# Performance work log

Measured on AMD Instinct MI355X. Metric: run time of the kernel, lower is better.

The kernel has to match this reference:

```python
import jax, jax.numpy as jnp
import numpy as np

PC_MIN = jnp.array([0.0, -39.68, -3.0], jnp.float32)
VOX = jnp.array([0.16, 0.16, 4.0], jnp.float32)
NX, NY = 432, 496  # grid cells in x and y (z grid size is 1)
MAXP = 32          # max points per pillar


def setup_inputs():
    key = jax.random.key(0)
    ks = jax.random.split(key, 16)
    B, N = 2, 16000
    u = jax.random.uniform(ks[0], (B, N, 4), dtype=jnp.float32)
    # points uniformly spread over the point-cloud range, intensity in [0,1)
    points = jnp.stack([u[..., 0] * 69.12, u[..., 1] * 79.36 - 39.68,
                        u[..., 2] * 4.0 - 3.0, u[..., 3]], axis=-1)

    def cw(k, co, ci):
        return jax.random.normal(k, (co, ci, 3, 3), jnp.float32) / np.float32(np.sqrt(ci * 9.0))

    def cws(k, L, c):
        return jax.random.normal(k, (L, c, c, 3, 3), jnp.float32) / np.float32(np.sqrt(c * 9.0))

    def st(k, shape):
        k1, k2 = jax.random.split(k)
        return (1.0 + 0.1 * jax.random.normal(k1, shape, jnp.float32),
                0.1 * jax.random.normal(k2, shape, jnp.float32))

    vfe_w = 0.1 * jax.random.normal(ks[1], (64, 10), jnp.float32)
    vfe_s, vfe_t = st(ks[2], (64,))
    b1_w0 = cw(ks[3], 4, 64);   b1_s0, b1_t0 = st(ks[4], (4,))
    b1_w = cws(ks[5], 3, 4);    b1_s, b1_t = st(ks[6], (3, 4))
    b2_w0 = cw(ks[7], 16, 4);   b2_s0, b2_t0 = st(ks[8], (16,))
    b2_w = cws(ks[9], 5, 16);   b2_s, b2_t = st(ks[10], (5, 16))
    b3_w0 = cw(ks[11], 64, 16); b3_s0, b3_t0 = st(ks[12], (64,))
    b3_w = cws(ks[13], 5, 64);  b3_s, b3_t = st(ks[14], (5, 64))
    return dict(points=points, vfe_w=vfe_w, vfe_s=vfe_s, vfe_t=vfe_t,
                b1_w0=b1_w0, b1_s0=b1_s0, b1_t0=b1_t0, b1_w=b1_w, b1_s=b1_s, b1_t=b1_t,
                b2_w0=b2_w0, b2_s0=b2_s0, b2_t0=b2_t0, b2_w=b2_w, b2_s=b2_s, b2_t=b2_t,
                b3_w0=b3_w0, b3_s0=b3_s0, b3_t0=b3_t0, b3_w=b3_w, b3_s=b3_s, b3_t=b3_t)


def _voxelize_vfe_scatter(points, vfe_w, vfe_s, vfe_t):
    """Hard voxelization (hash-bucket by pillar coord, pad to MAXP) + PillarVFE + scatter to BEV canvas."""
    B, N, C = points.shape
    V = B * N  # worst case: every point its own pillar
    pts = points.reshape(V, C)
    cid = jnp.floor((pts[:, :3] - PC_MIN) / VOX).astype(jnp.int32)
    cid = jnp.clip(cid, 0, jnp.array([NX - 1, NY - 1, 0], jnp.int32))
    bidx = jnp.repeat(jnp.arange(B, dtype=jnp.int32), N)
    # linear pillar id: b*NY*NX + y*NX + x  (z grid dim is 1 -> z idx always 0)
    gid = bidx * (NY * NX) + cid[:, 1] * NX + cid[:, 0]
    order = jnp.argsort(gid)  # stable -> preserves per-pillar point order
    g = gid[order]; p = pts[order]; c = cid[order]
    pos = jnp.arange(V, dtype=jnp.int32)
    flag = jnp.concatenate([jnp.ones((1,), bool), g[1:] != g[:-1]])
    vidx = jnp.cumsum(flag) - 1                                 # dense pillar index
    rank = pos - jax.lax.cummax(jnp.where(flag, pos, 0), axis=0)  # slot within pillar
    keep = rank < MAXP
    voxels = jnp.zeros((V, MAXP, C), points.dtype).at[vidx, rank].set(p, mode='drop')
    num = jnp.zeros((V,), jnp.int32).at[vidx].add(keep.astype(jnp.int32))
    OOB = B * NY * NX
    pillar_gid = jnp.full((V,), OOB, jnp.int32).at[vidx].set(g)  # unused slots stay out-of-bounds
    pillar_c = jnp.zeros((V, 3), jnp.int32).at[vidx].set(c)
    # PillarVFE features: [x,y,z,r, cluster offset(3), center offset(3)] = 10
    denom = jnp.maximum(num, 1).astype(points.dtype)[:, None]
    mean = jnp.zeros((V, 3), points.dtype).at[vidx].add(p[:, :3] * keep[:, None]) / denom
    f_cluster = voxels[:, :, :3] - mean[:, None, :]
    center = pillar_c.astype(points.dtype) * VOX + (VOX * 0.5 + PC_MIN)
    f_center = voxels[:, :, :3] - center[:, None, :]
    mask = (jnp.arange(MAXP)[None, :] < num[:, None])[:, :, None].astype(points.dtype)
    feat = jnp.concatenate([voxels, f_cluster, f_center], axis=-1) * mask  # (V, 32, 10)
    x = jnp.einsum('vpc,oc->vpo', feat, vfe_w)        # PFN linear (no bias)
    x = jax.nn.relu(x * vfe_s + vfe_t)                # eval-mode BN folded to scale/shift
    pillar = x.max(axis=1)                            # (V, 64) max over points
    canvas = jnp.zeros((B * NY * NX, 64), points.dtype).at[pillar_gid].set(pillar, mode='drop')
    return canvas.reshape(B, NY, NX, 64).transpose(0, 3, 1, 2)  # (B, 64, NY, NX)


def _conv_bn_relu(x, w, s, t):
    y = jax.lax.conv_general_dilated(x, w, (1, 1), [(1, 1), (1, 1)],
                                     dimension_numbers=('NCHW', 'OIHW', 'NCHW'))
    return jax.nn.relu(y * s[None, :, None, None] + t[None, :, None, None])


def _block(x, w0, s0, t0, ws, ss, ts):
    x = _conv_bn_relu(x, w0, s0, t0)
    for i in range(ws.shape[0]):  # fixed small layer count
        x = _conv_bn_relu(x, ws[i], ss[i], ts[i])
    return x


def reference(points, vfe_w, vfe_s, vfe_t,
              b1_w0, b1_s0, b1_t0, b1_w, b1_s, b1_t,
              b2_w0, b2_s0, b2_t0, b2_w, b2_s, b2_t,
              b3_w0, b3_s0, b3_t0, b3_w, b3_s, b3_t):
    bev = _voxelize_vfe_scatter(points, vfe_w, vfe_s, vfe_t)
    x1 = _block(bev, b1_w0, b1_s0, b1_t0, b1_w, b1_s, b1_t)
    x2 = _block(x1, b2_w0, b2_s0, b2_t0, b2_w, b2_s, b2_t)
    x3 = _block(x2, b3_w0, b3_s0, b3_t0, b3_w, b3_s, b3_t)
    # no deblocks (cfg lacks UPSAMPLE_STRIDES) -> concat raw block outputs: 4+16+64 = 84 ch
    return jnp.concatenate([x1, x2, x3], axis=1)  # (B, 84, 496, 432)
```

## Files before the change

### kernel.cpp

```cpp
#include <hip/hip_runtime.h>
#include <math.h>

static constexpr int H = 496, W = 432, Bn = 2, Np = 16000;
static constexpr int HW = H * W;

typedef __bf16 bf16x8 __attribute__((ext_vector_type(8)));
typedef float f32x16 __attribute__((ext_vector_type(16)));

__device__ inline void bin_xy(float px, float py, int& ix, int& iy) {
  ix = (int)floorf(px * 6.25f);
  iy = (int)floorf((py + 39.68f) * 6.25f);
  ix = min(max(ix, 0), W - 1);
  iy = min(max(iy, 0), H - 1);
}

__global__ __launch_bounds__(256)
void count_kernel(const float* __restrict__ pts, int* __restrict__ cnt,
                  float* __restrict__ sums) {
  int p = blockIdx.x * blockDim.x + threadIdx.x;
  if (p >= Bn * Np) return;
  float px = pts[p * 4 + 0], py = pts[p * 4 + 1], pz = pts[p * 4 + 2];
  int b = p / Np;
  int ix, iy;
  bin_xy(px, py, ix, iy);
  int gid = b * HW + iy * W + ix;
  atomicAdd(&cnt[gid], 1);
  atomicAdd(&sums[3 * gid + 0], px);
  atomicAdd(&sums[3 * gid + 1], py);
  atomicAdd(&sums[3 * gid + 2], pz);
}

__global__ __launch_bounds__(256)
void vfe_kernel(const float* __restrict__ pts, const int* __restrict__ cnt,
                const float* __restrict__ sums, const float* __restrict__ vw,
                const float* __restrict__ vs, const float* __restrict__ vt,
                float* __restrict__ canv) {
  int tid = blockIdx.x * blockDim.x + threadIdx.x;
  if (tid >= Bn * Np * 64) return;
  int o = tid & 63;
  int p = tid >> 6;
  int b = p / Np;
  float px = pts[p * 4 + 0], py = pts[p * 4 + 1];
  float pz = pts[p * 4 + 2], pr = pts[p * 4 + 3];
  int ix, iy;
  bin_xy(px, py, ix, iy);
  int gid = b * HW + iy * W + ix;
  int n = cnt[gid];
  float denom = (float)max(n, 1);
  float mx = sums[3 * gid + 0] / denom;
  float my = sums[3 * gid + 1] / denom;
  float mz = sums[3 * gid + 2] / denom;
  float cx = (float)ix * 0.16f + 0.08f;
  float cy = (float)iy * 0.16f + (0.08f - 39.68f);
  float f[10] = {px, py, pz, pr, px - mx, py - my, pz - mz,
                 px - cx, py - cy, pz + 1.0f};
  const float* wr = vw + o * 10;
  float d = 0.f;
#pragma unroll
  for (int c = 0; c < 10; c++) d += f[c] * wr[c];
  float val = d * vs[o] + vt[o];
  val = fmaxf(val, 0.f);
  if (n < 32) val = fmaxf(val, fmaxf(vt[o], 0.f));
  unsigned int* dst = (unsigned int*)(canv + (size_t)gid * 64 + o);
  atomicMax(dst, __float_as_uint(val));
}

__global__ __launch_bounds__(256)
void conv64_nhwc(const float* __restrict__ canv, const float* __restrict__ w0,
                 const float* __restrict__ s, const float* __restrict__ t,
                 float* __restrict__ out4) {
  int pix = blockIdx.x * 256 + threadIdx.x;
  if (pix >= Bn * HW) return;
  int b = pix / HW;
  int rem = pix - b * HW;
  int y = rem / W;
  int x = rem - y * W;
  const float* cb = canv + (size_t)b * HW * 64;
  float a0 = 0.f, a1 = 0.f, a2 = 0.f, a3 = 0.f;
#pragma unroll
  for (int ky = 0; ky < 3; ky++) {
    int yy = y + ky - 1;
    if ((unsigned)yy >= (unsigned)H) continue;
#pragma unroll
    for (int kx = 0; kx < 3; kx++) {
      int xx = x + kx - 1;
      if ((unsigned)xx >= (unsigned)W) continue;
      const float* cp = cb + (size_t)(yy * W + xx) * 64;
      const float* wp = w0 + (ky * 3 + kx);
#pragma unroll
      for (int c4 = 0; c4 < 16; c4++) {
        float4 v = *(const float4*)(cp + c4 * 4);
        int ci = c4 * 4;
        a0 = fmaf(v.x, wp[0 * 576 + (ci + 0) * 9], a0);
        a1 = fmaf(v.x, wp[1 * 576 + (ci + 0) * 9], a1);
        a2 = fmaf(v.x, wp[2 * 576 + (ci + 0) * 9], a2);
        a3 = fmaf(v.x, wp[3 * 576 + (ci + 0) * 9], a3);
        a0 = fmaf(v.y, wp[0 * 576 + (ci + 1) * 9], a0);
        a1 = fmaf(v.y, wp[1 * 576 + (ci + 1) * 9], a1);
        a2 = fmaf(v.y, wp[2 * 576 + (ci + 1) * 9], a2);
        a3 = fmaf(v.y, wp[3 * 576 + (ci + 1) * 9], a3);
        a0 = fmaf(v.z, wp[0 * 576 + (ci + 2) * 9], a0);
        a1 = fmaf(v.z, wp[1 * 576 + (ci + 2) * 9], a1);
        a2 = fmaf(v.z, wp[2 * 576 + (ci + 2) * 9], a2);
        a3 = fmaf(v.z, wp[3 * 576 + (ci + 2) * 9], a3);
        a0 = fmaf(v.w, wp[0 * 576 + (ci + 3) * 9], a0);
        a1 = fmaf(v.w, wp[1 * 576 + (ci + 3) * 9], a1);
        a2 = fmaf(v.w, wp[2 * 576 + (ci + 3) * 9], a2);
        a3 = fmaf(v.w, wp[3 * 576 + (ci + 3) * 9], a3);
      }
    }
  }
  float* ob = out4 + (size_t)b * 4 * HW + rem;
  ob[0 * HW] = fmaxf(a0 * s[0] + t[0], 0.f);
  ob[1 * HW] = fmaxf(a1 * s[1] + t[1], 0.f);
  ob[2 * HW] = fmaxf(a2 * s[2] + t[2], 0.f);
  ob[3 * HW] = fmaxf(a3 * s[3] + t[3], 0.f);
}

template <int CI, int COT>
__global__ __launch_bounds__(256)
void conv3x3(const float* __restrict__ in, int in_bs, const float* __restrict__ w,
             const float* __restrict__ s, const float* __restrict__ t,
             float* __restrict__ out, int out_bs, int npix) {
  int pix = blockIdx.x * blockDim.x + threadIdx.x;
  if (pix >= npix) return;
  int b = pix / HW;
  int rem = pix - b * HW;
  int y = rem / W;
  int x = rem - y * W;
  int co0 = blockIdx.y * COT;
  const float* inb = in + (size_t)b * in_bs;

  int offs[9];
  bool okm[9];
#pragma unroll
  for (int ky = 0; ky < 3; ky++) {
    int yy = y + ky - 1;
    bool yok = (unsigned)yy < (unsigned)H;
#pragma unroll
    for (int kx = 0; kx < 3; kx++) {
      int xx = x + kx - 1;
      okm[ky * 3 + kx] = yok && ((unsigned)xx < (unsigned)W);
      offs[ky * 3 + kx] = yy * W + xx;
    }
  }
  float acc[COT];
#pragma unroll
  for (int i = 0; i < COT; i++) acc[i] = 0.f;
  for (int ci = 0; ci < CI; ci++) {
    const float* ip = inb + (size_t)ci * HW;
    float iv[9];
#pragma unroll
    for (int k = 0; k < 9; k++) iv[k] = okm[k] ? ip[offs[k]] : 0.f;
    const float* wp = w + ((size_t)co0 * CI + ci) * 9;
#pragma unroll
    for (int cg_ = 0; cg_ < COT; cg_++) {
      const float* wc = wp + (size_t)cg_ * CI * 9;
#pragma unroll
      for (int k = 0; k < 9; k++) acc[cg_] = fmaf(iv[k], wc[k], acc[cg_]);
    }
  }
  float* ob = out + (size_t)b * out_bs + (size_t)rem;
#pragma unroll
  for (int cg_ = 0; cg_ < COT; cg_++) {
    float v = acc[cg_] * s[co0 + cg_] + t[co0 + cg_];
    ob[(size_t)(co0 + cg_) * HW] = fmaxf(v, 0.f);
  }
}

__global__ __launch_bounds__(256)
void conv16_dual(const float* __restrict__ in, const float* __restrict__ w,
                 const float* __restrict__ s, const float* __restrict__ t,
                 float* __restrict__ out, __bf16* __restrict__ n16) {
  int pix = blockIdx.x * blockDim.x + threadIdx.x;
  if (pix >= Bn * HW) return;
  int b = pix / HW;
  int rem = pix - b * HW;
  int y = rem / W;
  int x = rem - y * W;
  const float* inb = in + (size_t)b * 16 * HW;

  int offs[9];
  bool okm[9];
#pragma unroll
  for (int ky = 0; ky < 3; ky++) {
    int yy = y + ky - 1;
    bool yok = (unsigned)yy < (unsigned)H;
#pragma unroll
    for (int kx = 0; kx < 3; kx++) {
      int xx = x + kx - 1;
      okm[ky * 3 + kx] = yok && ((unsigned)xx < (unsigned)W);
      offs[ky * 3 + kx] = yy * W + xx;
    }
  }
  float acc[16];
#pragma unroll
  for (int i = 0; i < 16; i++) acc[i] = 0.f;
  for (int ci = 0; ci < 16; ci++) {
    const float* ip = inb + (size_t)ci * HW;
    float iv[9];
#pragma unroll
    for (int k = 0; k < 9; k++) iv[k] = okm[k] ? ip[offs[k]] : 0.f;
    const float* wp = w + (size_t)ci * 9;
#pragma unroll
    for (int cg_ = 0; cg_ < 16; cg_++) {
      const float* wc = wp + (size_t)cg_ * 16 * 9;
#pragma unroll
      for (int k = 0; k < 9; k++) acc[cg_] = fmaf(iv[k], wc[k], acc[cg_]);
    }
  }
  float* ob = out + (size_t)b * 84 * HW + (size_t)rem;
  __bf16 vv[16];
#pragma unroll
  for (int cg_ = 0; cg_ < 16; cg_++) {
    float v = fmaxf(acc[cg_] * s[cg_] + t[cg_], 0.f);
    ob[(size_t)cg_ * HW] = v;
    vv[cg_] = (__bf16)v;
  }
  __bf16* nb = n16 + (size_t)b * (84 * HW * 2) + (size_t)rem * 16;
  *(bf16x8*)nb = *(bf16x8*)vv;
  *(bf16x8*)(nb + 8) = *(bf16x8*)(vv + 8);
}

__global__ __launch_bounds__(256)
void prepack(const float* __restrict__ w0, const float* __restrict__ ws,
             __bf16* __restrict__ wt) {
  int idx = blockIdx.x * 256 + threadIdx.x;
  const int E0 = 64 * 144, EN = 64 * 576;
  if (idx < E0) {
    int blk = idx >> 9, rem = idx & 511;
    int tp = blk >> 1, nt = blk & 1;
    int co = nt * 32 + (rem >> 4);
    int ci = rem & 15;
    int ky = tp / 3, kx = tp - ky * 3;
    wt[idx] = (__bf16)w0[((co * 16 + ci) * 3 + ky) * 3 + kx];
  } else {
    int j = idx - E0;
    if (j >= 5 * EN) return;
    int n = j / EN, rr = j - n * EN;
    int blk = rr >> 9, rem = rr & 511;
    int tpkc = blk >> 1, nt = blk & 1;
    int tp = tpkc >> 2, kc = tpkc & 3;
    int co = nt * 32 + (rem >> 4);
    int ci = kc * 16 + (rem & 15);
    int ky = tp / 3, kx = tp - ky * 3;
    wt[idx] = (__bf16)ws[n * 36864 + ((co * 64 + ci) * 3 + ky) * 3 + kx];
  }
}

template <int CI, bool FINAL>
__global__ __launch_bounds__(256, 3)
void mconv(const __bf16* __restrict__ in, size_t in_bstride,
           const __bf16* __restrict__ wt, const float* __restrict__ s,
           const float* __restrict__ t, __bf16* __restrict__ outb,
           size_t outb_bstride, float* __restrict__ outf, size_t outf_bstride) {
  constexpr int KC = CI / 16;
  constexpr int PADW = (CI == 64) ? 72 : 24;
  constexpr int HALO_B = 324 * PADW * 2;
  constexpr int TRAN_B = FINAL ? 128 * 66 * 4 : 0;
  constexpr int SMEM_B = HALO_B > TRAN_B ? HALO_B : TRAN_B;
  __shared__ __align__(16) char smem[SMEM_B];
  __bf16* hl = (__bf16*)smem;

  const int tid = threadIdx.x;
  const int bz = blockIdx.y;
  const int ty = blockIdx.x / 27, tx = blockIdx.x - ty * 27;
  const int y0 = ty * 16, x0 = tx * 16;
  in += (size_t)bz * in_bstride;

  constexpr int NCH = CI / 8;
  constexpr int TOT = 324 * NCH;
  for (int q = tid; q < TOT; q += 256) {
    int hp = q / NCH, c8 = q - hp * NCH;
    int hy = hp / 18, hx = hp - hy * 18;
    int gy = y0 - 1 + hy, gx = x0 - 1 + hx;
    int4 v = {0, 0, 0, 0};
    if ((unsigned)gy < (unsigned)H && (unsigned)gx < (unsigned)W)
      v = *(const int4*)(in + (size_t)(gy * W + gx) * CI + c8 * 8);
    *(int4*)(hl + hp * PADW + c8 * 8) = v;
  }
  __syncthreads();

  const int lane = tid & 63;
  const int wv = tid >> 6;
  const int col = lane & 31, half = lane >> 5;
  const int ly0 = 4 * wv + (col >> 4);
  const int lx = col & 15;

  f32x16 z = {0.f, 0.f, 0.f, 0.f, 0.f, 0.f, 0.f, 0.f,
              0.f, 0.f, 0.f, 0.f, 0.f, 0.f, 0.f, 0.f};
  f32x16 a00 = z, a01 = z, a10 = z, a11 = z;

  const int laneoff = col * 16 + half * 8;
  const __bf16* wbase = wt + laneoff;

#pragma unroll
  for (int tp = 0; tp < 9; ++tp) {
    const __bf16* a0r = hl + ((ly0 + tp / 3) * 18 + lx + tp % 3) * PADW + half * 8;
    const __bf16* a1r = a0r + 2 * 18 * PADW;
    const __bf16* bb = wbase + ((tp * KC) << 10);
#pragma unroll
    for (int kc = 0; kc < KC; ++kc) {
      bf16x8 af0 = *(const bf16x8*)(a0r + kc * 16);
      bf16x8 af1 = *(const bf16x8*)(a1r + kc * 16);
      bf16x8 b0 = *(const bf16x8*)(bb + (kc << 10));
      bf16x8 b1 = *(const bf16x8*)(bb + (kc << 10) + 512);
      a00 = __builtin_amdgcn_mfma_f32_32x32x16_bf16(af0, b0, a00, 0, 0, 0);
      a01 = __builtin_amdgcn_mfma_f32_32x32x16_bf16(af0, b1, a01, 0, 0, 0);
      a10 = __builtin_amdgcn_mfma_f32_32x32x16_bf16(af1, b0, a10, 0, 0, 0);
      a11 = __builtin_amdgcn_mfma_f32_32x32x16_bf16(af1, b1, a11, 0, 0, 0);
    }
  }

  float s0 = s[col], t0v = t[col], s1 = s[col + 32], t1v = t[col + 32];
  if constexpr (!FINAL) {
    __bf16* ob = outb + (size_t)bz * outb_bstride;
#pragma unroll
    for (int r = 0; r < 16; ++r) {
      int row = (r & 3) + 8 * (r >> 2) + 4 * half;
      int py = y0 + 4 * wv + (row >> 4);
      int px = x0 + (row & 15);
      size_t gp0 = (size_t)py * W + px;
      size_t gp1 = gp0 + (size_t)2 * W;
      ob[gp0 * 64 + col] = (__bf16)fmaxf(a00[r] * s0 + t0v, 0.f);
      ob[gp0 * 64 + col + 32] = (__bf16)fmaxf(a01[r] * s1 + t1v, 0.f);
      ob[gp1 * 64 + col] = (__bf16)fmaxf(a10[r] * s0 + t0v, 0.f);
      ob[gp1 * 64 + col + 32] = (__bf16)fmaxf(a11[r] * s1 + t1v, 0.f);
    }
  } else {
    float* of = outf + (size_t)bz * outf_bstride;
    float* tl = (float*)smem;
    for (int h = 0; h < 2; ++h) {
      __syncthreads();
      if ((wv >> 1) == h) {
        int wl = wv & 1;
#pragma unroll
        for (int r = 0; r < 16; ++r) {
          int row = (r & 3) + 8 * (r >> 2) + 4 * half;
          int lp0 = (4 * wl + (row >> 4)) * 16 + (row & 15);
          int lp1 = lp0 + 32;
          tl[lp0 * 66 + col] = fmaxf(a00[r] * s0 + t0v, 0.f);
          tl[lp0 * 66 + col + 32] = fmaxf(a01[r] * s1 + t1v, 0.f);
          tl[lp1 * 66 + col] = fmaxf(a10[r] * s0 + t0v, 0.f);
          tl[lp1 * 66 + col + 32] = fmaxf(a11[r] * s1 + t1v, 0.f);
        }
      }
      __syncthreads();
      for (int e = tid; e < 128 * 64; e += 256) {
        int co = e >> 7, mtl = e & 127;
        of[(size_t)co * HW + (size_t)(y0 + h * 8 + (mtl >> 4)) * W +
           (x0 + (mtl & 15))] = tl[mtl * 66 + co];
      }
    }
  }
}

extern "C" void kernel_launch(void* const* d_in, const int* in_sizes, int n_in,
                              void* d_out, int out_size, void* d_ws, size_t ws_size,
                              hipStream_t stream) {
  const float* pts  = (const float*)d_in[0];
  const float* vw   = (const float*)d_in[1];
  const float* vs   = (const float*)d_in[2];
  const float* vt   = (const float*)d_in[3];
  const float* b1w0 = (const float*)d_in[4];
  const float* b1s0 = (const float*)d_in[5];
  const float* b1t0 = (const float*)d_in[6];
  const float* b1w  = (const float*)d_in[7];
  const float* b1s  = (const float*)d_in[8];
  const float* b1t  = (const float*)d_in[9];
  const float* b2w0 = (const float*)d_in[10];
  const float* b2s0 = (const float*)d_in[11];
  const float* b2t0 = (const float*)d_in[12];
  const float* b2w  = (const float*)d_in[13];
  const float* b2s  = (const float*)d_in[14];
  const float* b2t  = (const float*)d_in[15];
  const float* b3w0 = (const float*)d_in[16];
  const float* b3s0 = (const float*)d_in[17];
  const float* b3t0 = (const float*)d_in[18];
  const float* b3w  = (const float*)d_in[19];
  const float* b3s  = (const float*)d_in[20];
  const float* b3t  = (const float*)d_in[21];
  float* out = (float*)d_out;

  float* wsf = (float*)d_ws;
  int* cnt = (int*)wsf;
  float* sums = wsf + (size_t)2 * HW;
  float* s16a = wsf;
  float* s16b = wsf + (size_t)32 * HW;
  float* canv = wsf + (size_t)64 * HW;
  __bf16* ppA = (__bf16*)d_ws;
  __bf16* Wt = (__bf16*)((char*)d_ws + (size_t)192 * HW * 4);

  prepack<<<756, 256, 0, stream>>>(b3w0, b3w, Wt);

  hipMemsetAsync(cnt, 0, (size_t)8 * HW * sizeof(float), stream);
  hipMemsetAsync(canv, 0, (size_t)128 * HW * sizeof(float), stream);

  count_kernel<<<(Bn * Np + 255) / 256, 256, 0, stream>>>(pts, cnt, sums);
  vfe_kernel<<<(Bn * Np * 64 + 255) / 256, 256, 0, stream>>>(pts, cnt, sums, vw, vs,
                                                             vt, canv);

  const int g2 = (2 * HW + 255) / 256;
  dim3 blk(256);

  conv64_nhwc<<<g2, blk, 0, stream>>>(canv, b1w0, b1s0, b1t0, s16a);
  conv3x3<4, 4><<<dim3(g2, 1), blk, 0, stream>>>(s16a, 4 * HW, b1w + 0 * 144,
                                                 b1s + 0, b1t + 0, s16b, 4 * HW,
                                                 2 * HW);
  conv3x3<4, 4><<<dim3(g2, 1), blk, 0, stream>>>(s16b, 4 * HW, b1w + 1 * 144,
                                                 b1s + 4, b1t + 4, s16a, 4 * HW,
                                                 2 * HW);
  conv3x3<4, 4><<<dim3(g2, 1), blk, 0, stream>>>(s16a, 4 * HW, b1w + 2 * 144,
                                                 b1s + 8, b1t + 8, out, 84 * HW,
                                                 2 * HW);

  __bf16* n16 = (__bf16*)(out + (size_t)20 * HW);
  conv3x3<4, 16><<<dim3(g2, 1), blk, 0, stream>>>(out, 84 * HW, b2w0, b2s0, b2t0,
                                                  s16a, 16 * HW, 2 * HW);
  conv3x3<16, 16><<<dim3(g2, 1), blk, 0, stream>>>(s16a, 16 * HW, b2w + 0 * 2304,
                                                   b2s + 0, b2t + 0, s16b, 16 * HW,
                                                   2 * HW);
  conv3x3<16, 16><<<dim3(g2, 1), blk, 0, stream>>>(s16b, 16 * HW, b2w + 1 * 2304,
                                                   b2s + 16, b2t + 16, s16a, 16 * HW,
                                                   2 * HW);
  conv3x3<16, 16><<<dim3(g2, 1), blk, 0, stream>>>(s16a, 16 * HW, b2w + 2 * 2304,
                                                   b2s + 32, b2t + 32, s16b, 16 * HW,
                                                   2 * HW);
  conv3x3<16, 16><<<dim3(g2, 1), blk, 0, stream>>>(s16b, 16 * HW, b2w + 3 * 2304,
                                                   b2s + 48, b2t + 48, s16a, 16 * HW,
                                                   2 * HW);
  conv16_dual<<<g2, blk, 0, stream>>>(s16a, b2w + 4 * 2304, b2s + 64, b2t + 64,
                                      out + 4 * HW, n16);

  const size_t canv_s = (size_t)84 * HW * 2;
  const size_t ppa_s = (size_t)64 * HW;
  dim3 mg(31 * 27, Bn);
  mconv<16, false><<<mg, blk, 0, stream>>>(n16, canv_s, Wt, b3s0, b3t0, ppA, ppa_s,
                                           nullptr, 0);
  mconv<64, false><<<mg, blk, 0, stream>>>(ppA, ppa_s, Wt + 9216 + 0 * 36864,
                                           b3s + 0, b3t + 0, n16, canv_s, nullptr,
                                           0);
  mconv<64, false><<<mg, blk, 0, stream>>>(n16, canv_s, Wt + 9216 + 1 * 36864,
                                           b3s + 64, b3t + 64, ppA, ppa_s, nullptr,
                                           0);
  mconv<64, false><<<mg, blk, 0, stream>>>(ppA, ppa_s, Wt + 9216 + 2 * 36864,
                                           b3s + 128, b3t + 128, n16, canv_s,
                                           nullptr, 0);
  mconv<64, false><<<mg, blk, 0, stream>>>(n16, canv_s, Wt + 9216 + 3 * 36864,
                                           b3s + 192, b3t + 192, ppA, ppa_s,
                                           nullptr, 0);
  mconv<64, true><<<mg, blk, 0, stream>>>(ppA, ppa_s, Wt + 9216 + 4 * 36864,
                                          b3s + 256, b3t + 256, nullptr, 0,
                                          out + (size_t)20 * HW, (size_t)84 * HW);
}
```

Baseline: 909.6 us.

## Tile first 64-channel conv with shared-memory halo and split output channels

```diff
diff --git a/kernel.cpp b/kernel.cpp
--- a/kernel.cpp
+++ b/kernel.cpp
@@ -66,55 +66,59 @@
 }
 
 __global__ __launch_bounds__(256)
-void conv64_nhwc(const float* __restrict__ canv, const float* __restrict__ w0,
+void conv64_tile(const float* __restrict__ canv, const float* __restrict__ w0,
                  const float* __restrict__ s, const float* __restrict__ t,
                  float* __restrict__ out4) {
-  int pix = blockIdx.x * 256 + threadIdx.x;
-  if (pix >= Bn * HW) return;
-  int b = pix / HW;
-  int rem = pix - b * HW;
-  int y = rem / W;
-  int x = rem - y * W;
+  constexpr int PADP = 68;
+  __shared__ __align__(16) float hl[180 * PADP];
+
+  const int tid = threadIdx.x;
+  const int b = blockIdx.y;
+  const int ty = blockIdx.x / 27, tx = blockIdx.x - ty * 27;
+  const int y0 = ty * 8, x0 = tx * 16;
   const float* cb = canv + (size_t)b * HW * 64;
-  float a0 = 0.f, a1 = 0.f, a2 = 0.f, a3 = 0.f;
+
+  for (int q = tid; q < 180 * 16; q += 256) {
+    int hp = q >> 4, c4 = q & 15;
+    int hy = hp / 18, hx = hp - hy * 18;
+    int gy = y0 - 1 + hy, gx = x0 - 1 + hx;
+    float4 v = {0.f, 0.f, 0.f, 0.f};
+    if ((unsigned)gy < (unsigned)H && (unsigned)gx < (unsigned)W)
+      v = *(const float4*)(cb + (size_t)(gy * W + gx) * 64 + c4 * 4);
+    *(float4*)(hl + hp * PADP + c4 * 4) = v;
+  }
+  __syncthreads();
+
+  const int p = tid >> 1, hf = tid & 1;
+  const int ly = p >> 4, lx = p & 15;
+  const int co = hf * 2;
+  float a0 = 0.f, a1 = 0.f;
+  const float* wb = w0 + (size_t)co * 576;
+
 #pragma unroll
   for (int ky = 0; ky < 3; ky++) {
-    int yy = y + ky - 1;
-    if ((unsigned)yy >= (unsigned)H) continue;
 #pragma unroll
     for (int kx = 0; kx < 3; kx++) {
-      int xx = x + kx - 1;
-      if ((unsigned)xx >= (unsigned)W) continue;
-      const float* cp = cb + (size_t)(yy * W + xx) * 64;
-      const float* wp = w0 + (ky * 3 + kx);
+      const float* hp_ = hl + ((ly + ky) * 18 + lx + kx) * PADP;
+      const float* wp = wb + (ky * 3 + kx);
 #pragma unroll
       for (int c4 = 0; c4 < 16; c4++) {
-        float4 v = *(const float4*)(cp + c4 * 4);
+        float4 v = *(const float4*)(hp_ + c4 * 4);
         int ci = c4 * 4;
-        a0 = fmaf(v.x, wp[0 * 576 + (ci + 0) * 9], a0);
-        a1 = fmaf(v.x, wp[1 * 576 + (ci + 0) * 9], a1);
-        a2 = fmaf(v.x, wp[2 * 576 + (ci + 0) * 9], a2);
-        a3 = fmaf(v.x, wp[3 * 576 + (ci + 0) * 9], a3);
-        a0 = fmaf(v.y, wp[0 * 576 + (ci + 1) * 9], a0);
-        a1 = fmaf(v.y, wp[1 * 576 + (ci + 1) * 9], a1);
-        a2 = fmaf(v.y, wp[2 * 576 + (ci + 1) * 9], a2);
-        a3 = fmaf(v.y, wp[3 * 576 + (ci + 1) * 9], a3);
-        a0 = fmaf(v.z, wp[0 * 576 + (ci + 2) * 9], a0);
-        a1 = fmaf(v.z, wp[1 * 576 + (ci + 2) * 9], a1);
-        a2 = fmaf(v.z, wp[2 * 576 + (ci + 2) * 9], a2);
-        a3 = fmaf(v.z, wp[3 * 576 + (ci + 2) * 9], a3);
-        a0 = fmaf(v.w, wp[0 * 576 + (ci + 3) * 9], a0);
-        a1 = fmaf(v.w, wp[1 * 576 + (ci + 3) * 9], a1);
-        a2 = fmaf(v.w, wp[2 * 576 + (ci + 3) * 9], a2);
-        a3 = fmaf(v.w, wp[3 * 576 + (ci + 3) * 9], a3);
+        a0 = fmaf(v.x, wp[(ci + 0) * 9], a0);
+        a1 = fmaf(v.x, wp[576 + (ci + 0) * 9], a1);
+        a0 = fmaf(v.y, wp[(ci + 1) * 9], a0);
+        a1 = fmaf(v.y, wp[576 + (ci + 1) * 9], a1);
+        a0 = fmaf(v.z, wp[(ci + 2) * 9], a0);
+        a1 = fmaf(v.z, wp[576 + (ci + 2) * 9], a1);
+        a0 = fmaf(v.w, wp[(ci + 3) * 9], a0);
+        a1 = fmaf(v.w, wp[576 + (ci + 3) * 9], a1);
       }
     }
   }
-  float* ob = out4 + (size_t)b * 4 * HW + rem;
-  ob[0 * HW] = fmaxf(a0 * s[0] + t[0], 0.f);
-  ob[1 * HW] = fmaxf(a1 * s[1] + t[1], 0.f);
-  ob[2 * HW] = fmaxf(a2 * s[2] + t[2], 0.f);
-  ob[3 * HW] = fmaxf(a3 * s[3] + t[3], 0.f);
+  float* ob = out4 + (size_t)b * 4 * HW + (size_t)(y0 + ly) * W + x0 + lx;
+  ob[(size_t)co * HW] = fmaxf(a0 * s[co] + t[co], 0.f);
+  ob[(size_t)(co + 1) * HW] = fmaxf(a1 * s[co + 1] + t[co + 1], 0.f);
 }
 
 template <int CI, int COT>
@@ -403,7 +407,7 @@
   const int g2 = (2 * HW + 255) / 256;
   dim3 blk(256);
 
-  conv64_nhwc<<<g2, blk, 0, stream>>>(canv, b1w0, b1s0, b1t0, s16a);
+  conv64_tile<<<dim3(27 * 62, Bn), blk, 0, stream>>>(canv, b1w0, b1s0, b1t0, s16a);
   conv3x3<4, 4><<<dim3(g2, 1), blk, 0, stream>>>(s16a, 4 * HW, b1w + 0 * 144,
                                                  b1s + 0, b1t + 0, s16b, 4 * HW,
                                                  2 * HW);
```

After: 1.342 ms. 47.5% more time.
